# Kernel optimization log

Hardware: AMD Instinct MI355X
Metric: run time of the kernel (lower is better)

## Reference

```python
import jax, jax.numpy as jnp
import numpy as np

K_PERIODS = 4   # k_periods
PMAX = 64       # pmax
MIN_P = 16      # min_period_threshold (already clamped to <= PMAX)


def setup_inputs() -> dict:
    key = jax.random.key(0)
    B, T, N = 32, 512, 128
    x = jax.random.normal(key, (B, T, N), dtype=jnp.float32)
    return {"x": x}


def reference(x):
    # x: [B, T, N]
    B, T, N = x.shape
    K = K_PERIODS
    seqs = jnp.transpose(x, (0, 2, 1)).reshape(B * N, T)  # [BN, T]

    # top-k nonzero frequencies by rFFT amplitude
    spec = jnp.fft.rfft(seqs, axis=-1)                    # [BN, T//2+1]
    amp = jnp.abs(spec)
    amp = amp.at[..., 0].set(0.0)                         # zero DC component
    kamp, kidx = jax.lax.top_k(amp, K)                    # [BN, K] each
    kidx = jnp.maximum(kidx, 1)

    # periods and cycle counts
    P = jnp.clip(T // kidx, MIN_P, PMAX)                  # [BN, K]
    cycles = jnp.maximum(T // P, 1)                       # [BN, K]
    take = cycles * P

    # static upper bound on cycles (torch uses data-dependent cycles.max();
    # extra trailing cycle slots here are fully masked to zero)
    Cmax = T // MIN_P
    idx_c = jnp.arange(Cmax)                              # [Cmax]
    idx_p = jnp.arange(PMAX)                              # [Pmax]

    base = jnp.maximum(T - take, 0)[..., None, None]      # [BN, K, 1, 1]
    indices = base + idx_c[None, None, :, None] * P[..., None, None] \
              + idx_p[None, None, None, :]                # [BN, K, Cmax, Pmax]
    indices = jnp.clip(indices, 0, T - 1)

    # gather: broadcast seqs over (K, Cmax)
    gathered = jnp.take_along_axis(seqs[:, None, None, :], indices, axis=-1)

    mask = ((idx_c[None, None, :, None] < cycles[..., None, None]) &
            (idx_p[None, None, None, :] < P[..., None, None])).astype(x.dtype)
    gathered = gathered * mask

    gathered = gathered.reshape(B, N, K, Cmax, PMAX)
    mask = mask.reshape(B, N, K, Cmax, PMAX)
    kamp = kamp.reshape(B, N, K)
    return gathered, mask, kamp
```

## Files before the change

kernel.cpp:

```cpp
#include <hip/hip_runtime.h>
#include <math.h>

#define TLEN 512
#define NCH  128
#define KP   4
#define PMAXV 64
#define CMAXV 32
#define MINP 16
#define NSEQ 4096
#define OUTG ((size_t)NSEQ * KP * CMAXV * PMAXV)

#define PAD(i) ((i) + ((i) >> 4))

typedef float nfloat4 __attribute__((ext_vector_type(4)));

__global__ void twiddle_setup(double2* __restrict__ Wg) {
    const int j = threadIdx.x;
    double ang = -6.283185307179586476925286766559 * (double)j / (double)TLEN;
    double sv, cv;
    sincos(ang, &sv, &cv);
    Wg[j] = make_double2(cv, sv);
}

__global__ __launch_bounds__(256) void periodicity_kernel(
    const float* __restrict__ x,
    const double2* __restrict__ Wg,
    float* __restrict__ out_g,
    float* __restrict__ out_m,
    float* __restrict__ out_a)
{
    const int s    = blockIdx.x;
    const int tid  = threadIdx.x;
    const int lane = tid & 63;
    const int wave = tid >> 6;

    __shared__ float   seqf[TLEN];
    __shared__ double2 X[TLEN + (TLEN >> 4)];
    __shared__ double2 W[256 + 16];
    __shared__ double  amp2[280];
    __shared__ double  bestv[KP];
    __shared__ int     besti[KP];
    __shared__ int     Ps[KP], Cs[KP], Bs[KP];

    const int b = s >> 7;
    const int n = s & (NCH - 1);
    const float* col = x + (size_t)b * TLEN * NCH + n;
    for (int i = tid; i < TLEN; i += 256)
        seqf[i] = col[(size_t)i * NCH];
    {
        double2 w = Wg[tid];
        W[PAD(tid)] = w;
    }
    __syncthreads();

    {
        const int base = wave << 7;
        int i0 = base + lane, i1 = base + 64 + lane;
        int r0 = (int)(__brev((unsigned)i0) >> 23);
        int r1 = (int)(__brev((unsigned)i1) >> 23);
        X[PAD(i0)] = make_double2((double)seqf[r0], 0.0);
        X[PAD(i1)] = make_double2((double)seqf[r1], 0.0);
    }
    __builtin_amdgcn_wave_barrier();

    #pragma unroll
    for (int st = 1; st <= 7; ++st) {
        const int half = 1 << (st - 1);
        const int pos  = tid & (half - 1);
        const int i1   = ((tid >> (st - 1)) << st) + pos;
        const int i2   = i1 + half;
        const double2 wv = W[PAD(pos << (9 - st))];
        const double2 a  = X[PAD(i1)];
        const double2 c  = X[PAD(i2)];
        const double tr = wv.x * c.x - wv.y * c.y;
        const double ti = wv.x * c.y + wv.y * c.x;
        X[PAD(i1)] = make_double2(a.x + tr, a.y + ti);
        X[PAD(i2)] = make_double2(a.x - tr, a.y - ti);
        __builtin_amdgcn_wave_barrier();
    }

    #pragma unroll
    for (int st = 8; st <= 9; ++st) {
        __syncthreads();
        const int half = 1 << (st - 1);
        const int pos  = tid & (half - 1);
        const int i1   = ((tid >> (st - 1)) << st) + pos;
        const int i2   = i1 + half;
        const double2 wv = W[PAD(pos << (9 - st))];
        const double2 a  = X[PAD(i1)];
        const double2 c  = X[PAD(i2)];
        const double tr = wv.x * c.x - wv.y * c.y;
        const double ti = wv.x * c.y + wv.y * c.x;
        X[PAD(i1)] = make_double2(a.x + tr, a.y + ti);
        X[PAD(i2)] = make_double2(a.x - tr, a.y - ti);
    }
    __syncthreads();

    {
        double2 v = X[PAD(tid)];
        amp2[PAD(tid)] = (tid == 0) ? 0.0 : (v.x * v.x + v.y * v.y);
        if (tid == 0) {
            double2 vn = X[PAD(TLEN / 2)];
            amp2[PAD(TLEN / 2)] = vn.x * vn.x + vn.y * vn.y;
        }
    }
    __syncthreads();

    if (wave == 0) {
        for (int q = 0; q < KP; ++q) {
            double v  = amp2[PAD(lane)];
            int    vi = lane;
            #pragma unroll
            for (int j = 1; j < 4; ++j) {
                double u = amp2[PAD(lane + 64 * j)];
                if (u > v) { v = u; vi = lane + 64 * j; }
            }
            if (lane == 0) {
                double u = amp2[PAD(256)];
                if (u > v) { v = u; vi = 256; }
            }
            #pragma unroll
            for (int off = 32; off > 0; off >>= 1) {
                double ov = __shfl_xor(v, off, 64);
                int    oi = __shfl_xor(vi, off, 64);
                if (ov > v || (ov == v && oi < vi)) { v = ov; vi = oi; }
            }
            if (lane == 0) {
                bestv[q] = v;
                besti[q] = vi;
                amp2[PAD(vi)] = -1.0;
            }
            __builtin_amdgcn_wave_barrier();
        }
        if (lane < KP) {
            int ki = besti[lane];
            if (ki < 1) ki = 1;
            int P = TLEN / ki;
            P = P < MINP ? MINP : (P > PMAXV ? PMAXV : P);
            int cyc = TLEN / P;
            Ps[lane] = P;
            Cs[lane] = cyc;
            Bs[lane] = TLEN - cyc * P;
            out_a[(size_t)s * KP + lane] = (float)sqrt(bestv[lane]);
        }
    }
    __syncthreads();

    float* og = out_g + (size_t)s * (KP * CMAXV * PMAXV);
    float* om = out_m + (size_t)s * (KP * CMAXV * PMAXV);
    const int pp = (tid & 15) << 2;
    for (int r = tid >> 4; r < KP * CMAXV; r += 16) {
        const int k = r >> 5;
        const int c = r & (CMAXV - 1);
        const int P = Ps[k], cyc = Cs[k], base = Bs[k];
        nfloat4 g = (nfloat4)(0.f, 0.f, 0.f, 0.f);
        nfloat4 m = (nfloat4)(0.f, 0.f, 0.f, 0.f);
        if (c < cyc) {
            const int idx = base + c * P + pp;
            if (pp     < P) { g.x = seqf[idx];     m.x = 1.f; }
            if (pp + 1 < P) { g.y = seqf[idx + 1]; m.y = 1.f; }
            if (pp + 2 < P) { g.z = seqf[idx + 2]; m.z = 1.f; }
            if (pp + 3 < P) { g.w = seqf[idx + 3]; m.w = 1.f; }
        }
        __builtin_nontemporal_store(g, (nfloat4*)(og + r * PMAXV + pp));
        __builtin_nontemporal_store(m, (nfloat4*)(om + r * PMAXV + pp));
    }
}

extern "C" void kernel_launch(void* const* d_in, const int* in_sizes, int n_in,
                              void* d_out, int out_size, void* d_ws, size_t ws_size,
                              hipStream_t stream) {
    const float* x = (const float*)d_in[0];
    float* out = (float*)d_out;
    float* og = out;
    float* om = out + OUTG;
    float* oa = om + OUTG;
    double2* Wg = (double2*)d_ws;

    twiddle_setup<<<dim3(1), dim3(256), 0, stream>>>(Wg);
    periodicity_kernel<<<dim3(NSEQ), dim3(256), 0, stream>>>(x, Wg, og, om, oa);
}
```

Baseline: 287.9 us.

## Split FFT/top-k parameter stage from output writer into separate kernels

Splits the fused kernel in two. The first kernel computes the FFT, top-k, period parameters and amplitudes, and stages each transposed sequence plus its parameters in workspace. A second, lightweight kernel reloads them and streams out the gathered and mask tensors, so the write-heavy phase runs with low LDS use and can reach higher occupancy. The cost is an extra launch, a round trip of the sequences through global memory, and the loss of the overlap that came from the fused blocks mixing compute and stores.

```diff
diff --git a/kernel.cpp b/kernel.cpp
--- a/kernel.cpp
+++ b/kernel.cpp
@@ -22,11 +22,11 @@
     Wg[j] = make_double2(cv, sv);
 }
 
-__global__ __launch_bounds__(256) void periodicity_kernel(
+__global__ __launch_bounds__(256) void param_kernel(
     const float* __restrict__ x,
     const double2* __restrict__ Wg,
-    float* __restrict__ out_g,
-    float* __restrict__ out_m,
+    float* __restrict__ seq_ws,
+    int4*  __restrict__ prm_ws,
     float* __restrict__ out_a)
 {
     const int s    = blockIdx.x;
@@ -40,18 +40,17 @@
     __shared__ double  amp2[280];
     __shared__ double  bestv[KP];
     __shared__ int     besti[KP];
-    __shared__ int     Ps[KP], Cs[KP], Bs[KP];
 
     const int b = s >> 7;
     const int n = s & (NCH - 1);
     const float* col = x + (size_t)b * TLEN * NCH + n;
     for (int i = tid; i < TLEN; i += 256)
         seqf[i] = col[(size_t)i * NCH];
-    {
-        double2 w = Wg[tid];
-        W[PAD(tid)] = w;
-    }
-    __syncthreads();
+    W[PAD(tid)] = Wg[tid];
+    __syncthreads();
+
+    for (int i = tid; i < TLEN; i += 256)
+        seq_ws[(size_t)s * TLEN + i] = seqf[i];
 
     {
         const int base = wave << 7;
@@ -138,17 +137,36 @@
             int P = TLEN / ki;
             P = P < MINP ? MINP : (P > PMAXV ? PMAXV : P);
             int cyc = TLEN / P;
-            Ps[lane] = P;
-            Cs[lane] = cyc;
-            Bs[lane] = TLEN - cyc * P;
+            prm_ws[(size_t)s * KP + lane] = make_int4(P, cyc, TLEN - cyc * P, 0);
             out_a[(size_t)s * KP + lane] = (float)sqrt(bestv[lane]);
         }
+    }
+}
+
+__global__ __launch_bounds__(256) void writer_kernel(
+    const float* __restrict__ seq_ws,
+    const int4*  __restrict__ prm_ws,
+    float* __restrict__ out_g,
+    float* __restrict__ out_m)
+{
+    const int s   = blockIdx.x;
+    const int tid = threadIdx.x;
+
+    __shared__ float seqf[TLEN];
+    __shared__ int   Ps[KP], Cs[KP], Bs[KP];
+
+    if (tid < TLEN / 4)
+        ((nfloat4*)seqf)[tid] = ((const nfloat4*)(seq_ws + (size_t)s * TLEN))[tid];
+    if (tid < KP) {
+        int4 p = prm_ws[(size_t)s * KP + tid];
+        Ps[tid] = p.x; Cs[tid] = p.y; Bs[tid] = p.z;
     }
     __syncthreads();
 
     float* og = out_g + (size_t)s * (KP * CMAXV * PMAXV);
     float* om = out_m + (size_t)s * (KP * CMAXV * PMAXV);
     const int pp = (tid & 15) << 2;
+    #pragma unroll
     for (int r = tid >> 4; r < KP * CMAXV; r += 16) {
         const int k = r >> 5;
         const int c = r & (CMAXV - 1);
@@ -175,8 +193,13 @@
     float* og = out;
     float* om = out + OUTG;
     float* oa = om + OUTG;
-    double2* Wg = (double2*)d_ws;
+
+    char* ws = (char*)d_ws;
+    double2* Wg   = (double2*)ws;
+    float*  seqw  = (float*)(ws + 8192);
+    int4*   prmw  = (int4*)(ws + 8192 + (size_t)NSEQ * TLEN * 4);
 
     twiddle_setup<<<dim3(1), dim3(256), 0, stream>>>(Wg);
-    periodicity_kernel<<<dim3(NSEQ), dim3(256), 0, stream>>>(x, Wg, og, om, oa);
-}
+    param_kernel<<<dim3(NSEQ), dim3(256), 0, stream>>>(x, Wg, seqw, prmw, oa);
+    writer_kernel<<<dim3(NSEQ), dim3(256), 0, stream>>>(seqw, prmw, og, om);
+}
```

After: 302.3 us. 1.05x slower.

## Process four sequences per block with one wave per sequence FFT

Applied to the files above, without the earlier changes.

Each block now handles four adjacent channels, one wavefront each, so the 512-point FFT, top-k selection and output writes of a sequence run within a single wave using only wave barriers instead of block-wide syncs. The input load reads four contiguous channels per time step, and the FFT data moves to split real/imaginary arrays with a different padding. Top-k results stay in registers rather than shared memory, and the output stores switch from nontemporal to regular stores. The cost is four times more FFT work per wave, more LDS per block and fewer blocks in flight.

```diff
diff --git a/kernel.cpp b/kernel.cpp
--- a/kernel.cpp
+++ b/kernel.cpp
@@ -10,7 +10,9 @@
 #define NSEQ 4096
 #define OUTG ((size_t)NSEQ * KP * CMAXV * PMAXV)
 
-#define PAD(i) ((i) + ((i) >> 4))
+#define PAD8(i) ((i) + ((i) >> 3))
+#define XP   580
+#define SEQP 520
 
 typedef float nfloat4 __attribute__((ext_vector_type(4)));
 
@@ -29,141 +31,147 @@
     float* __restrict__ out_m,
     float* __restrict__ out_a)
 {
-    const int s    = blockIdx.x;
     const int tid  = threadIdx.x;
     const int lane = tid & 63;
-    const int wave = tid >> 6;
+    const int w    = tid >> 6;
+    const int s0   = blockIdx.x << 2;
+    const int b    = s0 >> 7;
+    const int n0   = s0 & (NCH - 1);
 
-    __shared__ float   seqf[TLEN];
-    __shared__ double2 X[TLEN + (TLEN >> 4)];
-    __shared__ double2 W[256 + 16];
-    __shared__ double  amp2[280];
-    __shared__ double  bestv[KP];
-    __shared__ int     besti[KP];
-    __shared__ int     Ps[KP], Cs[KP], Bs[KP];
+    __shared__ float   seqf[4 * SEQP];
+    __shared__ double  re[4 * XP];
+    __shared__ double  im[4 * XP];
+    __shared__ double2 W[256];
 
-    const int b = s >> 7;
-    const int n = s & (NCH - 1);
-    const float* col = x + (size_t)b * TLEN * NCH + n;
-    for (int i = tid; i < TLEN; i += 256)
-        seqf[i] = col[(size_t)i * NCH];
     {
-        double2 w = Wg[tid];
-        W[PAD(tid)] = w;
+        const int col = tid & 3;
+        const int t0  = tid >> 2;
+        const float* base = x + (size_t)b * TLEN * NCH + n0 + col;
+        #pragma unroll
+        for (int it = 0; it < 8; ++it) {
+            const int t = t0 + 64 * it;
+            seqf[col * SEQP + t] = base[(size_t)t * NCH];
+        }
+        W[tid] = Wg[tid];
     }
     __syncthreads();
 
-    {
-        const int base = wave << 7;
-        int i0 = base + lane, i1 = base + 64 + lane;
-        int r0 = (int)(__brev((unsigned)i0) >> 23);
-        int r1 = (int)(__brev((unsigned)i1) >> 23);
-        X[PAD(i0)] = make_double2((double)seqf[r0], 0.0);
-        X[PAD(i1)] = make_double2((double)seqf[r1], 0.0);
+    float*  sf = seqf + w * SEQP;
+    double* RE = re + w * XP;
+    double* IM = im + w * XP;
+
+    #pragma unroll
+    for (int u = 0; u < 8; ++u) {
+        const int i = lane + 64 * u;
+        const int r = (int)(__brev((unsigned)i) >> 23);
+        RE[PAD8(i)] = (double)sf[r];
+        IM[PAD8(i)] = 0.0;
     }
     __builtin_amdgcn_wave_barrier();
 
-    #pragma unroll
-    for (int st = 1; st <= 7; ++st) {
+    for (int st = 1; st <= 9; ++st) {
         const int half = 1 << (st - 1);
-        const int pos  = tid & (half - 1);
-        const int i1   = ((tid >> (st - 1)) << st) + pos;
-        const int i2   = i1 + half;
-        const double2 wv = W[PAD(pos << (9 - st))];
-        const double2 a  = X[PAD(i1)];
-        const double2 c  = X[PAD(i2)];
-        const double tr = wv.x * c.x - wv.y * c.y;
-        const double ti = wv.x * c.y + wv.y * c.x;
-        X[PAD(i1)] = make_double2(a.x + tr, a.y + ti);
-        X[PAD(i2)] = make_double2(a.x - tr, a.y - ti);
+        #pragma unroll
+        for (int u = 0; u < 4; ++u) {
+            const int j   = lane + 64 * u;
+            const int pos = j & (half - 1);
+            const int i1  = ((j >> (st - 1)) << st) + pos;
+            const int i2  = i1 + half;
+            const double2 wv = W[pos << (9 - st)];
+            const double ar = RE[PAD8(i1)], ai = IM[PAD8(i1)];
+            const double cr = RE[PAD8(i2)], ci = IM[PAD8(i2)];
+            const double tr = wv.x * cr - wv.y * ci;
+            const double ti = wv.x * ci + wv.y * cr;
+            RE[PAD8(i1)] = ar + tr;  IM[PAD8(i1)] = ai + ti;
+            RE[PAD8(i2)] = ar - tr;  IM[PAD8(i2)] = ai - ti;
+        }
         __builtin_amdgcn_wave_barrier();
     }
 
     #pragma unroll
-    for (int st = 8; st <= 9; ++st) {
-        __syncthreads();
-        const int half = 1 << (st - 1);
-        const int pos  = tid & (half - 1);
-        const int i1   = ((tid >> (st - 1)) << st) + pos;
-        const int i2   = i1 + half;
-        const double2 wv = W[PAD(pos << (9 - st))];
-        const double2 a  = X[PAD(i1)];
-        const double2 c  = X[PAD(i2)];
-        const double tr = wv.x * c.x - wv.y * c.y;
-        const double ti = wv.x * c.y + wv.y * c.x;
-        X[PAD(i1)] = make_double2(a.x + tr, a.y + ti);
-        X[PAD(i2)] = make_double2(a.x - tr, a.y - ti);
+    for (int u = 0; u < 4; ++u) {
+        const int k = lane + 64 * u;
+        const double xr = RE[PAD8(k)], xi = IM[PAD8(k)];
+        RE[PAD8(k)] = (k == 0) ? 0.0 : (xr * xr + xi * xi);
     }
-    __syncthreads();
+    if (lane == 0) {
+        const double xr = RE[PAD8(256)], xi = IM[PAD8(256)];
+        RE[PAD8(256)] = xr * xr + xi * xi;
+    }
+    __builtin_amdgcn_wave_barrier();
 
+    double bv0, bv1, bv2, bv3;
+    int    bi0, bi1, bi2, bi3;
+    #pragma unroll
+    for (int q = 0; q < KP; ++q) {
+        double v  = RE[PAD8(lane)];
+        int    vi = lane;
+        #pragma unroll
+        for (int u = 1; u < 4; ++u) {
+            const double uu = RE[PAD8(lane + 64 * u)];
+            if (uu > v) { v = uu; vi = lane + 64 * u; }
+        }
+        if (lane == 0) {
+            const double uu = RE[PAD8(256)];
+            if (uu > v) { v = uu; vi = 256; }
+        }
+        #pragma unroll
+        for (int off = 32; off > 0; off >>= 1) {
+            const double ov = __shfl_xor(v, off, 64);
+            const int    oi = __shfl_xor(vi, off, 64);
+            if (ov > v || (ov == v && oi < vi)) { v = ov; vi = oi; }
+        }
+        if (q == 0) { bv0 = v; bi0 = vi; }
+        else if (q == 1) { bv1 = v; bi1 = vi; }
+        else if (q == 2) { bv2 = v; bi2 = vi; }
+        else { bv3 = v; bi3 = vi; }
+        if (lane == 0) RE[PAD8(vi)] = -1.0;
+        __builtin_amdgcn_wave_barrier();
+    }
+
+    int P0, P1, P2, P3, C0, C1, C2, C3, B0, B1, B2, B3;
     {
-        double2 v = X[PAD(tid)];
-        amp2[PAD(tid)] = (tid == 0) ? 0.0 : (v.x * v.x + v.y * v.y);
-        if (tid == 0) {
-            double2 vn = X[PAD(TLEN / 2)];
-            amp2[PAD(TLEN / 2)] = vn.x * vn.x + vn.y * vn.y;
-        }
+        int k0 = bi0 < 1 ? 1 : bi0;  P0 = TLEN / k0;
+        P0 = P0 < MINP ? MINP : (P0 > PMAXV ? PMAXV : P0);
+        C0 = TLEN / P0;  B0 = TLEN - C0 * P0;
+        int k1 = bi1 < 1 ? 1 : bi1;  P1 = TLEN / k1;
+        P1 = P1 < MINP ? MINP : (P1 > PMAXV ? PMAXV : P1);
+        C1 = TLEN / P1;  B1 = TLEN - C1 * P1;
+        int k2 = bi2 < 1 ? 1 : bi2;  P2 = TLEN / k2;
+        P2 = P2 < MINP ? MINP : (P2 > PMAXV ? PMAXV : P2);
+        C2 = TLEN / P2;  B2 = TLEN - C2 * P2;
+        int k3 = bi3 < 1 ? 1 : bi3;  P3 = TLEN / k3;
+        P3 = P3 < MINP ? MINP : (P3 > PMAXV ? PMAXV : P3);
+        C3 = TLEN / P3;  B3 = TLEN - C3 * P3;
     }
-    __syncthreads();
-
-    if (wave == 0) {
-        for (int q = 0; q < KP; ++q) {
-            double v  = amp2[PAD(lane)];
-            int    vi = lane;
-            #pragma unroll
-            for (int j = 1; j < 4; ++j) {
-                double u = amp2[PAD(lane + 64 * j)];
-                if (u > v) { v = u; vi = lane + 64 * j; }
-            }
-            if (lane == 0) {
-                double u = amp2[PAD(256)];
-                if (u > v) { v = u; vi = 256; }
-            }
-            #pragma unroll
-            for (int off = 32; off > 0; off >>= 1) {
-                double ov = __shfl_xor(v, off, 64);
-                int    oi = __shfl_xor(vi, off, 64);
-                if (ov > v || (ov == v && oi < vi)) { v = ov; vi = oi; }
-            }
-            if (lane == 0) {
-                bestv[q] = v;
-                besti[q] = vi;
-                amp2[PAD(vi)] = -1.0;
-            }
-            __builtin_amdgcn_wave_barrier();
-        }
-        if (lane < KP) {
-            int ki = besti[lane];
-            if (ki < 1) ki = 1;
-            int P = TLEN / ki;
-            P = P < MINP ? MINP : (P > PMAXV ? PMAXV : P);
-            int cyc = TLEN / P;
-            Ps[lane] = P;
-            Cs[lane] = cyc;
-            Bs[lane] = TLEN - cyc * P;
-            out_a[(size_t)s * KP + lane] = (float)sqrt(bestv[lane]);
-        }
+    const int s = s0 + w;
+    if (lane == 0) {
+        out_a[(size_t)s * KP + 0] = (float)sqrt(bv0);
+        out_a[(size_t)s * KP + 1] = (float)sqrt(bv1);
+        out_a[(size_t)s * KP + 2] = (float)sqrt(bv2);
+        out_a[(size_t)s * KP + 3] = (float)sqrt(bv3);
     }
-    __syncthreads();
 
     float* og = out_g + (size_t)s * (KP * CMAXV * PMAXV);
     float* om = out_m + (size_t)s * (KP * CMAXV * PMAXV);
-    const int pp = (tid & 15) << 2;
-    for (int r = tid >> 4; r < KP * CMAXV; r += 16) {
+    const int pp = (lane & 15) << 2;
+    for (int r = lane >> 4; r < KP * CMAXV; r += 4) {
         const int k = r >> 5;
         const int c = r & (CMAXV - 1);
-        const int P = Ps[k], cyc = Cs[k], base = Bs[k];
+        const int P    = k == 0 ? P0 : k == 1 ? P1 : k == 2 ? P2 : P3;
+        const int cyc  = k == 0 ? C0 : k == 1 ? C1 : k == 2 ? C2 : C3;
+        const int base = k == 0 ? B0 : k == 1 ? B1 : k == 2 ? B2 : B3;
         nfloat4 g = (nfloat4)(0.f, 0.f, 0.f, 0.f);
         nfloat4 m = (nfloat4)(0.f, 0.f, 0.f, 0.f);
         if (c < cyc) {
             const int idx = base + c * P + pp;
-            if (pp     < P) { g.x = seqf[idx];     m.x = 1.f; }
-            if (pp + 1 < P) { g.y = seqf[idx + 1]; m.y = 1.f; }
-            if (pp + 2 < P) { g.z = seqf[idx + 2]; m.z = 1.f; }
-            if (pp + 3 < P) { g.w = seqf[idx + 3]; m.w = 1.f; }
+            if (pp     < P) { g.x = sf[idx];     m.x = 1.f; }
+            if (pp + 1 < P) { g.y = sf[idx + 1]; m.y = 1.f; }
+            if (pp + 2 < P) { g.z = sf[idx + 2]; m.z = 1.f; }
+            if (pp + 3 < P) { g.w = sf[idx + 3]; m.w = 1.f; }
         }
-        __builtin_nontemporal_store(g, (nfloat4*)(og + r * PMAXV + pp));
-        __builtin_nontemporal_store(m, (nfloat4*)(om + r * PMAXV + pp));
+        *(nfloat4*)(og + r * PMAXV + pp) = g;
+        *(nfloat4*)(om + r * PMAXV + pp) = m;
     }
 }
 
@@ -178,5 +186,5 @@
     double2* Wg = (double2*)d_ws;
 
     twiddle_setup<<<dim3(1), dim3(256), 0, stream>>>(Wg);
-    periodicity_kernel<<<dim3(NSEQ), dim3(256), 0, stream>>>(x, Wg, og, om, oa);
+    periodicity_kernel<<<dim3(NSEQ / 4), dim3(256), 0, stream>>>(x, Wg, og, om, oa);
 }
```

New measurement: 276.9 us. -3.8%, faster.
